# Performance work log

Hardware: AMD Instinct MI355X
Metric: run time of the kernel (lower is better)

## Reference

```python
import jax, jax.numpy as jnp
import numpy as np
import math

HIDDEN = 8
HEADS = 2
HEAD_DIM = HIDDEN // HEADS  # 4
MAX_SEQ = 102
B, S = 4096, 102


def _rotary_cache(seq_len, head_dim):
    # Matches _create_rotary_embeddings: dim = head_dim//2, inv_freq over arange(0, dim, 2)
    pos = jnp.arange(seq_len, dtype=jnp.float32)
    dim = head_dim // 2
    inv_freq = 1.0 / (10000.0 ** (jnp.arange(0, dim, 2, dtype=jnp.float32) / dim))
    sinusoid = pos[:, None] * inv_freq[None, :]           # [seq, dim//2] -> [102, 1]
    return jnp.stack([jnp.sin(sinusoid), jnp.cos(sinusoid)], axis=0)  # [2, seq, 1]


def _apply_rotary(x, cos, sin):
    # x: [B, H, S, hd]; cos/sin: [2, S, 1] (faithful to the source's buggy unpack,
    # which broadcasts the stacked sin/cos pair across the H==2 head dim)
    x2 = jnp.stack([-x[..., 1::2], x[..., ::2]], axis=-1).reshape(x.shape)
    return x * cos + x2 * sin


def setup_inputs() -> dict:
    key = jax.random.key(0)
    kq, kk, kv, k1, k2, k3, k4 = jax.random.split(key, 7)
    scale = 1.0 / math.sqrt(HIDDEN)
    return {
        "query": jax.random.normal(kq, (B, S, HIDDEN), dtype=jnp.float32),
        "key": jax.random.normal(kk, (B, S, HIDDEN), dtype=jnp.float32),
        "value": jax.random.normal(kv, (B, S, HIDDEN), dtype=jnp.float32),
        "wq": jax.random.normal(k1, (HIDDEN, HIDDEN), dtype=jnp.float32) * scale,
        "wk": jax.random.normal(k2, (HIDDEN, HIDDEN), dtype=jnp.float32) * scale,
        "wv": jax.random.normal(k3, (HIDDEN, HIDDEN), dtype=jnp.float32) * scale,
        "wo": jax.random.normal(k4, (HIDDEN, HIDDEN), dtype=jnp.float32) * scale,
    }


def reference(query, key, value, wq, wk, wv, wo):
    b, sq, _ = query.shape
    sk = key.shape[1]
    # nn.Linear (no bias): y = x @ W^T
    q = query @ wq.T
    k = key @ wk.T
    v = value @ wv.T
    # b n (h d) -> b h n d
    def split_heads(t, s):
        return t.reshape(b, s, HEADS, HEAD_DIM).transpose(0, 2, 1, 3)
    q = split_heads(q, sq)
    k = split_heads(k, sk)
    v = split_heads(v, sk)
    cache = _rotary_cache(MAX_SEQ, HEAD_DIM)
    sin_t = cache[:, :sq]  # [2, sq, 1] (named 'sin' in source, holds stacked sin/cos)
    cos_t = cache[:, :sk]  # [2, sk, 1]
    q = _apply_rotary(q, cos_t, sin_t)
    k = _apply_rotary(k, cos_t, sin_t)
    scale = 1.0 / math.sqrt(HEAD_DIM)
    # chunk_size = min(sk, 1024) = sk -> single chunk == full softmax attention
    scores = jnp.einsum('bhqd,bhkd->bhqk', q, k) * scale  # [B, H, Sq, Sk]
    attn = jax.nn.softmax(scores, axis=-1)
    out = jnp.einsum('bhqk,bhkd->bhqd', attn, v)
    # b h n d -> b n (h d)
    out = out.transpose(0, 2, 1, 3).reshape(b, sq, HIDDEN)
    return out @ wo.T
```

## Files before the change

kernel.cpp:

```cpp
#include <hip/hip_runtime.h>

#define NB   4096
#define SS   102
#define SSP  104
#define HID  8
#define NH   2
#define HD   4
#define RS   0.72134752044448170368f

typedef float v2f __attribute__((ext_vector_type(2)));

__device__ __forceinline__ int PIDX(int r) { return (r & 7) * 13 + (r >> 3); }

template<int CTRL>
__device__ __forceinline__ float dppf(float x) {
    return __builtin_bit_cast(float,
        __builtin_amdgcn_mov_dpp(__builtin_bit_cast(int, x), CTRL, 0xF, 0xF, true));
}
template<int CTRL>
__device__ __forceinline__ v2f dpp2(v2f x) {
    v2f r; r.x = dppf<CTRL>(x.x); r.y = dppf<CTRL>(x.y); return r;
}

__device__ __forceinline__ void proj8(const float4& a0, const float4& a1,
                                      const float4& b0, const float4& b1,
                                      const float* __restrict__ W, v2f x[8]) {
    v2f in[8] = { {a0.x,b0.x},{a0.y,b0.y},{a0.z,b0.z},{a0.w,b0.w},
                  {a1.x,b1.x},{a1.y,b1.y},{a1.z,b1.z},{a1.w,b1.w} };
#pragma unroll
    for (int i = 0; i < 8; ++i) {
        v2f acc = in[0] * W[i*8+0];
#pragma unroll
        for (int j = 1; j < 8; ++j) acc += in[j] * W[i*8+j];
        x[i] = acc;
    }
}

__global__ __launch_bounds__(256) void mha_fused_kernel(
    const float* __restrict__ query, const float* __restrict__ key,
    const float* __restrict__ value, const float* __restrict__ wq,
    const float* __restrict__ wk, const float* __restrict__ wv,
    const float* __restrict__ wo, float* __restrict__ out)
{
    __shared__ float sQ[NH * 52 * 8];
    __shared__ float sK[NH * SSP * HD];
    __shared__ float sV[NH * SSP * HD];
    __shared__ float sC[NH * SSP * HD];

    const int t    = threadIdx.x;
    const int b    = blockIdx.x;
    const int wid  = t >> 6;
    const int lane = t & 63;

    float4 a0, a1, b0, b1;
    if (wid < 3 && lane < 51) {
        const float* src = (wid == 0) ? query : (wid == 1) ? key : value;
        const float4* s4 = (const float4*)(src + (size_t)b * (SS * HID));
        a0 = s4[4*lane]; a1 = s4[4*lane+1]; b0 = s4[4*lane+2]; b1 = s4[4*lane+3];
    }
    if (t >= 208) {
        const int z = t - 208;
        if (z < 16) {
            sQ[(z >> 3) * 416 + 408 + (z & 7)] = 0.f;
        } else {
            const int rem = z & 15;
            const int h = rem >> 3, r = SS + ((rem >> 2) & 1), d = rem & 3;
            float* dst = (z < 32) ? sK : sV;
            dst[(h * SSP + PIDX(r)) * HD + d] = 0.f;
        }
    }

    if (wid < 3 && lane < 51) {
        const int r0 = 2 * lane;
        v2f sn, cs;
        if (wid < 2) {
            const float f0 = (float)r0, f1 = (float)(r0 + 1);
            sn = (v2f){ __sinf(f0), __sinf(f1) };
            cs = (v2f){ __cosf(f0), __cosf(f1) };
            if (wid == 0) { sn *= RS; cs *= RS; }
        }
        v2f x[8];
        if (wid == 0)      proj8(a0, a1, b0, b1, wq, x);
        else if (wid == 1) proj8(a0, a1, b0, b1, wk, x);
        else               proj8(a0, a1, b0, b1, wv, x);

        if (wid < 2) {
            const v2f y0 = (x[0]-x[1])*sn, y1 = (x[1]+x[0])*sn;
            const v2f y2 = (x[2]-x[3])*sn, y3 = (x[3]+x[2])*sn;
            const v2f y4 = (x[4]-x[5])*cs, y5 = (x[5]+x[4])*cs;
            const v2f y6 = (x[6]-x[7])*cs, y7 = (x[7]+x[6])*cs;
            if (wid == 0) {
                const int p = lane;
                float4* d = (float4*)sQ;
                d[2*p]       = make_float4(y0.x, y0.y, y1.x, y1.y);
                d[2*p+1]     = make_float4(y2.x, y2.y, y3.x, y3.y);
                d[104+2*p]   = make_float4(y4.x, y4.y, y5.x, y5.y);
                d[104+2*p+1] = make_float4(y6.x, y6.y, y7.x, y7.y);
            } else {
                const int i0 = PIDX(r0), i1 = PIDX(r0 + 1);
                float4* d = (float4*)sK;
                d[i0]      = make_float4(y0.x, y1.x, y2.x, y3.x);
                d[SSP+i0]  = make_float4(y4.x, y5.x, y6.x, y7.x);
                d[i1]      = make_float4(y0.y, y1.y, y2.y, y3.y);
                d[SSP+i1]  = make_float4(y4.y, y5.y, y6.y, y7.y);
            }
        } else {
            const int i0 = PIDX(r0), i1 = PIDX(r0 + 1);
            float4* d = (float4*)sV;
            d[i0]      = make_float4(x[0].x, x[1].x, x[2].x, x[3].x);
            d[SSP+i0]  = make_float4(x[4].x, x[5].x, x[6].x, x[7].x);
            d[i1]      = make_float4(x[0].y, x[1].y, x[2].y, x[3].y);
            d[SSP+i1]  = make_float4(x[4].y, x[5].y, x[6].y, x[7].y);
        }
    }
    __syncthreads();

    const int qp = lane >> 2, w = lane & 3;
    if (qp < 13) {
        const int h  = wid >> 1;
        const int qh = wid & 1;
        const int p0 = qh * 26 + 2 * qp;
        v2f q[2][4];
        {
            const float4* Q4 = (const float4*)sQ + h * 104;
#pragma unroll
            for (int P = 0; P < 2; ++P) {
                const float4 f0 = Q4[2*(p0+P)];
                const float4 f1 = Q4[2*(p0+P)+1];
                q[P][0] = (v2f){f0.x, f0.y}; q[P][1] = (v2f){f0.z, f0.w};
                q[P][2] = (v2f){f1.x, f1.y}; q[P][3] = (v2f){f1.z, f1.w};
            }
        }
        v2f acc[2][4], l[2];
#pragma unroll
        for (int P = 0; P < 2; ++P) {
            l[P] = (v2f){0.f, 0.f};
#pragma unroll
            for (int d = 0; d < 4; ++d) acc[P][d] = (v2f){0.f, 0.f};
        }
        const float4* Ka = (const float4*)sK + h*SSP + 13*w;
        const float4* Kb = Ka + 52;
        const float4* Va = (const float4*)sV + h*SSP + 13*w;
        const float4* Vb = Va + 52;
#define BODY(KA, KB, VA, VB) { \
            _Pragma("unroll") \
            for (int P = 0; P < 2; ++P) { \
                v2f s = q[P][0]*(KA).x + q[P][1]*(KA).y + q[P][2]*(KA).z + q[P][3]*(KA).w; \
                v2f p; p.x = __builtin_amdgcn_exp2f(s.x); p.y = __builtin_amdgcn_exp2f(s.y); \
                l[P] += p; \
                acc[P][0] += p*(VA).x; acc[P][1] += p*(VA).y; \
                acc[P][2] += p*(VA).z; acc[P][3] += p*(VA).w; \
            } \
            _Pragma("unroll") \
            for (int P = 0; P < 2; ++P) { \
                v2f s = q[P][0]*(KB).x + q[P][1]*(KB).y + q[P][2]*(KB).z + q[P][3]*(KB).w; \
                v2f p; p.x = __builtin_amdgcn_exp2f(s.x); p.y = __builtin_amdgcn_exp2f(s.y); \
                l[P] += p; \
                acc[P][0] += p*(VB).x; acc[P][1] += p*(VB).y; \
                acc[P][2] += p*(VB).z; acc[P][3] += p*(VB).w; \
            } \
        }
        float4 cka = Ka[0], ckb = Kb[0], cva = Va[0], cvb = Vb[0];
        float4 nka = Ka[1], nkb = Kb[1], nva = Va[1], nvb = Vb[1];
#pragma unroll
        for (int j = 0; j < 13; ++j) {
            float4 fka, fkb, fva, fvb;
            if (j < 11) { fka = Ka[j+2]; fkb = Kb[j+2]; fva = Va[j+2]; fvb = Vb[j+2]; }
            BODY(cka, ckb, cva, cvb);
            cka = nka; ckb = nkb; cva = nva; cvb = nvb;
            if (j < 11) { nka = fka; nkb = fkb; nva = fva; nvb = fvb; }
        }
#undef BODY
        if (w >= 2) { l[0] -= (v2f){1.f, 1.f}; l[1] -= (v2f){1.f, 1.f}; }
#pragma unroll
        for (int P = 0; P < 2; ++P) {
            l[P] += dpp2<0xB1>(l[P]);
#pragma unroll
            for (int d = 0; d < 4; ++d) acc[P][d] += dpp2<0xB1>(acc[P][d]);
        }
#pragma unroll
        for (int P = 0; P < 2; ++P) {
            l[P] += dpp2<0x4E>(l[P]);
#pragma unroll
            for (int d = 0; d < 4; ++d) acc[P][d] += dpp2<0x4E>(acc[P][d]);
        }
        float4* comb = (float4*)sC + h * SSP;
#define WRITE_PAIR(P) { \
            const int r0 = 2 * (p0 + (P)); \
            if (r0 < SS) { \
                const float ix = 1.f / l[P].x; \
                comb[r0] = make_float4(acc[P][0].x*ix, acc[P][1].x*ix, \
                                       acc[P][2].x*ix, acc[P][3].x*ix); \
            } \
            if (r0 + 1 < SS) { \
                const float iy = 1.f / l[P].y; \
                comb[r0+1] = make_float4(acc[P][0].y*iy, acc[P][1].y*iy, \
                                         acc[P][2].y*iy, acc[P][3].y*iy); \
            } \
        }
        if      (w == 0) WRITE_PAIR(0)
        else if (w == 1) WRITE_PAIR(1)
#undef WRITE_PAIR
    }
    __syncthreads();

    const int row = wid * 26 + lane;
    if (lane < 26 && row < SS) {
        const float4 c0 = ((const float4*)sC)[row];
        const float4 c1 = ((const float4*)sC)[SSP + row];
        float o[8];
#pragma unroll
        for (int i = 0; i < 8; ++i) {
            const float* wr = wo + i*8;
            o[i] = c0.x*wr[0] + c0.y*wr[1] + c0.z*wr[2] + c0.w*wr[3]
                 + c1.x*wr[4] + c1.y*wr[5] + c1.z*wr[6] + c1.w*wr[7];
        }
        float4* o4 = (float4*)(out + (size_t)b * (SS * HID) + row * HID);
        o4[0] = make_float4(o[0], o[1], o[2], o[3]);
        o4[1] = make_float4(o[4], o[5], o[6], o[7]);
    }
}

extern "C" void kernel_launch(void* const* d_in, const int* in_sizes, int n_in,
                              void* d_out, int out_size, void* d_ws, size_t ws_size,
                              hipStream_t stream) {
    const float* query = (const float*)d_in[0];
    const float* key   = (const float*)d_in[1];
    const float* value = (const float*)d_in[2];
    const float* wq    = (const float*)d_in[3];
    const float* wk    = (const float*)d_in[4];
    const float* wv    = (const float*)d_in[5];
    const float* wo    = (const float*)d_in[6];
    float* out = (float*)d_out;
    mha_fused_kernel<<<NB, 256, 0, stream>>>(query, key, value, wq, wk, wv, wo, out);
}
```

Measured before the change: 141.0 us.

## Software-pipeline K/V LDS reads with inline asm and explicit lgkmcnt waits

Merges the K and V shared buffers into one array so a single base register with immediate offsets can address both. The attention loop is rewritten with inline-asm ds_read_b128 loads in a three-stage rotating buffer, with explicit s_waitcnt lgkmcnt and sched_barrier calls, so LDS reads overlap with the exp2/FMA work. The rotary sin/cos calls also switch from __sinf/__cosf to the precise sinf/cosf, which costs more instructions. Hand-placed waits bypass the compiler's scheduling and rely on the lgkm counter only tracking these reads, which is fragile.

```diff
diff --git a/kernel.cpp b/kernel.cpp
--- a/kernel.cpp
+++ b/kernel.cpp
@@ -6,9 +6,11 @@
 #define HID  8
 #define NH   2
 #define HD   4
+#define VOFF (NH * SSP * HD)
 #define RS   0.72134752044448170368f
 
 typedef float v2f __attribute__((ext_vector_type(2)));
+typedef float v4f __attribute__((ext_vector_type(4)));
 
 __device__ __forceinline__ int PIDX(int r) { return (r & 7) * 13 + (r >> 3); }
 
@@ -43,8 +45,7 @@
     const float* __restrict__ wo, float* __restrict__ out)
 {
     __shared__ float sQ[NH * 52 * 8];
-    __shared__ float sK[NH * SSP * HD];
-    __shared__ float sV[NH * SSP * HD];
+    __shared__ float sKV[2 * NH * SSP * HD];
     __shared__ float sC[NH * SSP * HD];
 
     const int t    = threadIdx.x;
@@ -65,8 +66,8 @@
         } else {
             const int rem = z & 15;
             const int h = rem >> 3, r = SS + ((rem >> 2) & 1), d = rem & 3;
-            float* dst = (z < 32) ? sK : sV;
-            dst[(h * SSP + PIDX(r)) * HD + d] = 0.f;
+            const int voff = (z < 32) ? 0 : VOFF;
+            sKV[voff + (h * SSP + PIDX(r)) * HD + d] = 0.f;
         }
     }
 
@@ -75,8 +76,8 @@
         v2f sn, cs;
         if (wid < 2) {
             const float f0 = (float)r0, f1 = (float)(r0 + 1);
-            sn = (v2f){ __sinf(f0), __sinf(f1) };
-            cs = (v2f){ __cosf(f0), __cosf(f1) };
+            sn = (v2f){ sinf(f0), sinf(f1) };
+            cs = (v2f){ cosf(f0), cosf(f1) };
             if (wid == 0) { sn *= RS; cs *= RS; }
         }
         v2f x[8];
@@ -98,7 +99,7 @@
                 d[104+2*p+1] = make_float4(y6.x, y6.y, y7.x, y7.y);
             } else {
                 const int i0 = PIDX(r0), i1 = PIDX(r0 + 1);
-                float4* d = (float4*)sK;
+                float4* d = (float4*)sKV;
                 d[i0]      = make_float4(y0.x, y1.x, y2.x, y3.x);
                 d[SSP+i0]  = make_float4(y4.x, y5.x, y6.x, y7.x);
                 d[i1]      = make_float4(y0.y, y1.y, y2.y, y3.y);
@@ -106,7 +107,7 @@
             }
         } else {
             const int i0 = PIDX(r0), i1 = PIDX(r0 + 1);
-            float4* d = (float4*)sV;
+            float4* d = (float4*)sKV + 208;
             d[i0]      = make_float4(x[0].x, x[1].x, x[2].x, x[3].x);
             d[SSP+i0]  = make_float4(x[4].x, x[5].x, x[6].x, x[7].x);
             d[i1]      = make_float4(x[0].y, x[1].y, x[2].y, x[3].y);
@@ -120,17 +121,36 @@
         const int h  = wid >> 1;
         const int qh = wid & 1;
         const int p0 = qh * 26 + 2 * qp;
+
+        const unsigned qb   = (unsigned)(size_t)&sQ[(h * 104 + 2 * p0) * 4];
+        const unsigned base = (unsigned)(size_t)&sKV[(h * SSP + 13 * w) * HD];
+
+        v4f qf0, qf1, qf2, qf3;
+        v4f s0Ka, s0Kb, s0Va, s0Vb;
+        v4f s1Ka, s1Kb, s1Va, s1Vb;
+        v4f s2Ka, s2Kb, s2Va, s2Vb;
+
+#define ISSUE(S, J) \
+    asm volatile("ds_read_b128 %0, %1 offset:%2" : "=v"(s##S##Ka) : "v"(base), "n"((J)*16));        \
+    asm volatile("ds_read_b128 %0, %1 offset:%2" : "=v"(s##S##Kb) : "v"(base), "n"(832 + (J)*16));  \
+    asm volatile("ds_read_b128 %0, %1 offset:%2" : "=v"(s##S##Va) : "v"(base), "n"(3328 + (J)*16)); \
+    asm volatile("ds_read_b128 %0, %1 offset:%2" : "=v"(s##S##Vb) : "v"(base), "n"(4160 + (J)*16))
+#define DSW8 asm volatile("s_waitcnt lgkmcnt(8)"); __builtin_amdgcn_sched_barrier(0)
+#define DSW4 asm volatile("s_waitcnt lgkmcnt(4)"); __builtin_amdgcn_sched_barrier(0)
+#define DSW0 asm volatile("s_waitcnt lgkmcnt(0)"); __builtin_amdgcn_sched_barrier(0)
+
+        asm volatile("ds_read_b128 %0, %1 offset:0"  : "=v"(qf0) : "v"(qb));
+        asm volatile("ds_read_b128 %0, %1 offset:16" : "=v"(qf1) : "v"(qb));
+        asm volatile("ds_read_b128 %0, %1 offset:32" : "=v"(qf2) : "v"(qb));
+        asm volatile("ds_read_b128 %0, %1 offset:48" : "=v"(qf3) : "v"(qb));
+        ISSUE(0, 0); ISSUE(1, 1);
+        DSW8;
         v2f q[2][4];
-        {
-            const float4* Q4 = (const float4*)sQ + h * 104;
-#pragma unroll
-            for (int P = 0; P < 2; ++P) {
-                const float4 f0 = Q4[2*(p0+P)];
-                const float4 f1 = Q4[2*(p0+P)+1];
-                q[P][0] = (v2f){f0.x, f0.y}; q[P][1] = (v2f){f0.z, f0.w};
-                q[P][2] = (v2f){f1.x, f1.y}; q[P][3] = (v2f){f1.z, f1.w};
-            }
-        }
+        q[0][0] = (v2f){qf0.x, qf0.y}; q[0][1] = (v2f){qf0.z, qf0.w};
+        q[0][2] = (v2f){qf1.x, qf1.y}; q[0][3] = (v2f){qf1.z, qf1.w};
+        q[1][0] = (v2f){qf2.x, qf2.y}; q[1][1] = (v2f){qf2.z, qf2.w};
+        q[1][2] = (v2f){qf3.x, qf3.y}; q[1][3] = (v2f){qf3.z, qf3.w};
+
         v2f acc[2][4], l[2];
 #pragma unroll
         for (int P = 0; P < 2; ++P) {
@@ -138,38 +158,37 @@
 #pragma unroll
             for (int d = 0; d < 4; ++d) acc[P][d] = (v2f){0.f, 0.f};
         }
-        const float4* Ka = (const float4*)sK + h*SSP + 13*w;
-        const float4* Kb = Ka + 52;
-        const float4* Va = (const float4*)sV + h*SSP + 13*w;
-        const float4* Vb = Va + 52;
-#define BODY(KA, KB, VA, VB) { \
-            _Pragma("unroll") \
-            for (int P = 0; P < 2; ++P) { \
-                v2f s = q[P][0]*(KA).x + q[P][1]*(KA).y + q[P][2]*(KA).z + q[P][3]*(KA).w; \
-                v2f p; p.x = __builtin_amdgcn_exp2f(s.x); p.y = __builtin_amdgcn_exp2f(s.y); \
-                l[P] += p; \
-                acc[P][0] += p*(VA).x; acc[P][1] += p*(VA).y; \
-                acc[P][2] += p*(VA).z; acc[P][3] += p*(VA).w; \
-            } \
-            _Pragma("unroll") \
-            for (int P = 0; P < 2; ++P) { \
-                v2f s = q[P][0]*(KB).x + q[P][1]*(KB).y + q[P][2]*(KB).z + q[P][3]*(KB).w; \
-                v2f p; p.x = __builtin_amdgcn_exp2f(s.x); p.y = __builtin_amdgcn_exp2f(s.y); \
-                l[P] += p; \
-                acc[P][0] += p*(VB).x; acc[P][1] += p*(VB).y; \
-                acc[P][2] += p*(VB).z; acc[P][3] += p*(VB).w; \
-            } \
-        }
-        float4 cka = Ka[0], ckb = Kb[0], cva = Va[0], cvb = Vb[0];
-        float4 nka = Ka[1], nkb = Kb[1], nva = Va[1], nvb = Vb[1];
-#pragma unroll
-        for (int j = 0; j < 13; ++j) {
-            float4 fka, fkb, fva, fvb;
-            if (j < 11) { fka = Ka[j+2]; fkb = Kb[j+2]; fva = Va[j+2]; fvb = Vb[j+2]; }
-            BODY(cka, ckb, cva, cvb);
-            cka = nka; ckb = nkb; cva = nva; cvb = nvb;
-            if (j < 11) { nka = fka; nkb = fkb; nva = fva; nvb = fvb; }
-        }
+
+#define HALF(KK, VV) { \
+    _Pragma("unroll") \
+    for (int P = 0; P < 2; ++P) { \
+        v2f sxy = q[P][0]*(KK).x + q[P][1]*(KK).y + q[P][2]*(KK).z + q[P][3]*(KK).w; \
+        v2f p; p.x = __builtin_amdgcn_exp2f(sxy.x); p.y = __builtin_amdgcn_exp2f(sxy.y); \
+        l[P] += p; \
+        acc[P][0] += p*(VV).x; acc[P][1] += p*(VV).y; \
+        acc[P][2] += p*(VV).z; acc[P][3] += p*(VV).w; \
+    } }
+#define BODY(S) HALF(s##S##Ka, s##S##Va) HALF(s##S##Kb, s##S##Vb)
+
+        ISSUE(2, 2);  DSW8; BODY(0);
+        ISSUE(0, 3);  DSW8; BODY(1);
+        ISSUE(1, 4);  DSW8; BODY(2);
+        ISSUE(2, 5);  DSW8; BODY(0);
+        ISSUE(0, 6);  DSW8; BODY(1);
+        ISSUE(1, 7);  DSW8; BODY(2);
+        ISSUE(2, 8);  DSW8; BODY(0);
+        ISSUE(0, 9);  DSW8; BODY(1);
+        ISSUE(1, 10); DSW8; BODY(2);
+        ISSUE(2, 11); DSW8; BODY(0);
+        ISSUE(0, 12); DSW8; BODY(1);
+                      DSW4; BODY(2);
+                      DSW0; BODY(0);
+
+#undef ISSUE
+#undef DSW8
+#undef DSW4
+#undef DSW0
+#undef HALF
 #undef BODY
         if (w >= 2) { l[0] -= (v2f){1.f, 1.f}; l[1] -= (v2f){1.f, 1.f}; }
 #pragma unroll
```

Result: faster. 129.8 us (-8.0%).
